# Performance work log

Measured on AMD Instinct MI355X. Metric: run time of the kernel, lower is better.

Reference implementation:

```python
import jax, jax.numpy as jnp
import numpy as np
from functools import partial

B, S, D, H, DK, DV, DFF = 4, 2048, 1024, 8, 128, 128, 4096
EPS = 1e-6

def rms_norm(x):
    return x * jax.lax.rsqrt(jnp.mean(x * x, axis=-1, keepdims=True) + EPS)

def l2norm(x):
    return x * jax.lax.rsqrt(jnp.sum(x * x, axis=-1, keepdims=True) + EPS)

def setup_inputs() -> dict:
    key = jax.random.key(0)
    ks = jax.random.split(key, 16)
    w = lambda k, shp: jax.random.normal(k, shp, dtype=jnp.float32) * 0.02
    return {
        'x': jax.random.normal(ks[0], (B, S, D), dtype=jnp.float32),
        'Wq': w(ks[1], (D, H * DK)),
        'Wk': w(ks[2], (D, H * DK)),
        'Wv': w(ks[3], (D, H * DV)),
        'Wb': w(ks[4], (D, H)),
        'Wa': w(ks[5], (D, H)),
        'A_log': jnp.log(jnp.linspace(1.0, 8.0, H).astype(jnp.float32)),
        'dt_bias': jax.random.normal(ks[6], (H,), dtype=jnp.float32) * 0.1,
        'Wg': w(ks[7], (D, H * DV)),
        'o_norm_w': jnp.ones((DV,), dtype=jnp.float32),
        'Wo': w(ks[8], (H * DV, D)),
        'W_fc': w(ks[9], (D, DFF)),
        'W_proj': w(ks[10], (DFF, D)),
    }

def gated_delta_net(h, Wq, Wk, Wv, Wb, Wa, A_log, dt_bias, Wg, o_norm_w, Wo):
    b, s, _ = h.shape
    q = l2norm(jax.nn.silu(h @ Wq).reshape(b, s, H, DK))
    k = l2norm(jax.nn.silu(h @ Wk).reshape(b, s, H, DK))
    v = jax.nn.silu(h @ Wv).reshape(b, s, H, DV)
    beta = jax.nn.sigmoid(h @ Wb)                                  # [b,s,H]
    g = -jnp.exp(A_log) * jax.nn.softplus(h @ Wa + dt_bias)       # [b,s,H]
    alpha = jnp.exp(g)
    scale = DK ** -0.5

    # time-major for scan
    tm = lambda a: jnp.moveaxis(a, 1, 0)
    qs, ks_, vs, als, bts = tm(q), tm(k), tm(v), tm(alpha), tm(beta)

    def step(Sst, inp):
        q_t, k_t, v_t, a_t, b_t = inp               # [b,H,dk],[b,H,dk],[b,H,dv],[b,H],[b,H]
        Sst = Sst * a_t[..., None, None]            # decay state [b,H,dk,dv]
        kv = jnp.einsum('bhd,bhde->bhe', k_t, Sst)  # current memory readout
        delta = (v_t - kv) * b_t[..., None]
        Sst = Sst + jnp.einsum('bhd,bhe->bhde', k_t, delta)
        o_t = jnp.einsum('bhd,bhde->bhe', q_t, Sst) * scale
        return Sst, o_t

    S0 = jnp.zeros((b, H, DK, DV), dtype=h.dtype)
    _, o = jax.lax.scan(step, S0, (qs, ks_, vs, als, bts))
    o = jnp.moveaxis(o, 0, 1)                       # [b,s,H,dv]

    gate = (h @ Wg).reshape(b, s, H, DV)
    o = rms_norm(o) * o_norm_w * jax.nn.silu(gate)  # gated RMSNorm
    return o.reshape(b, s, H * DV) @ Wo

def reference(x, Wq, Wk, Wv, Wb, Wa, A_log, dt_bias, Wg, o_norm_w, Wo, W_fc, W_proj):
    ln_scale = 1.0  # config.layer_norm_scaling = False
    h = gated_delta_net(ln_scale * rms_norm(x), Wq, Wk, Wv, Wb, Wa, A_log, dt_bias, Wg, o_norm_w, Wo)
    x = x + h
    m = ln_scale * rms_norm(x)
    y = jnp.square(jax.nn.relu(m @ W_fc)) @ W_proj  # nanoGPT ReLU^2 MLP
    return x + y
```

## Files before the change

### kernel.cpp

```cpp
#include <hip/hip_runtime.h>
#include <math.h>
#include <stdint.h>

#define ROWS 8192
#define DIM  1024
#define NH   8
#define DFF_ 4096
#define EPSF 1e-6f
#define SCALEQ 0.08838834764831845f

typedef __attribute__((ext_vector_type(8))) short short8;
typedef __attribute__((ext_vector_type(4))) float f32x4;

__device__ __forceinline__ float siluf(float x) {
    return x / (1.0f + expf(-x));
}
__device__ __forceinline__ unsigned short f2bf(float f) {
    uint32_t u = __float_as_uint(f);
    uint32_t r = (u + 0x7FFFu + ((u >> 16) & 1u)) >> 16;
    return (unsigned short)r;
}
__device__ __forceinline__ float bf2f(unsigned short u) {
    return __uint_as_float(((uint32_t)u) << 16);
}

__device__ __forceinline__ void async16(const void* g, void* l) {
    __builtin_amdgcn_global_load_lds(
        (const __attribute__((address_space(1))) uint32_t*)g,
        (__attribute__((address_space(3))) uint32_t*)l, 16, 0, 0);
}

__global__ void rmsnorm_bf16_kernel(const float* __restrict__ x, unsigned short* __restrict__ y) {
    int row = blockIdx.x;
    int tid = threadIdx.x;
    const float4* x4 = (const float4*)(x + (size_t)row * DIM);
    float4 v = x4[tid];
    float ss = v.x * v.x + v.y * v.y + v.z * v.z + v.w * v.w;
#pragma unroll
    for (int m = 1; m < 64; m <<= 1) ss += __shfl_xor(ss, m, 64);
    __shared__ float wss[4];
    if ((tid & 63) == 0) wss[tid >> 6] = ss;
    __syncthreads();
    float tot = wss[0] + wss[1] + wss[2] + wss[3];
    float r = rsqrtf(tot * (1.0f / 1024.0f) + EPSF);
    ushort4 o;
    o.x = f2bf(v.x * r); o.y = f2bf(v.y * r); o.z = f2bf(v.z * r); o.w = f2bf(v.w * r);
    ((ushort4*)(y + (size_t)row * DIM))[tid] = o;
}

__global__ void transpose_bf16_kernel(const float* __restrict__ W, unsigned short* __restrict__ WT,
                                      int K, int N) {
    __shared__ float tile[32][33];
    int n0 = blockIdx.x * 32, k0 = blockIdx.y * 32;
    int tx = threadIdx.x & 31, ty = threadIdx.x >> 5;
#pragma unroll
    for (int r = 0; r < 32; r += 8)
        tile[ty + r][tx] = W[(size_t)(k0 + ty + r) * N + n0 + tx];
    __syncthreads();
#pragma unroll
    for (int r = 0; r < 32; r += 8)
        WT[(size_t)(n0 + ty + r) * K + k0 + tx] = f2bf(tile[tx][ty + r]);
}

template <int EPI, typename CT>
__global__ __launch_bounds__(256) void mfma_gemm(
    const unsigned short* __restrict__ A, const unsigned short* __restrict__ BT,
    CT* __restrict__ C, const float* __restrict__ res, int M, int N, int K) {
    __shared__ __align__(16) unsigned short As[128 * 32];
    __shared__ __align__(16) unsigned short Bs[128 * 32];
    int tid = threadIdx.x;
    int w = tid >> 6, lane = tid & 63;

    int nwgx = gridDim.x;
    int nwg = nwgx * gridDim.y;
    int id = blockIdx.y * nwgx + blockIdx.x;
    int cpx = nwg >> 3;
    int nid = (id & 7) * cpx + (id >> 3);
    int bxs = nid % nwgx, bys = nid / nwgx;

    int bm = bys * 128, bn = bxs * 128;
    int wm = (w >> 1) * 64, wn = (w & 1) * 64;

    int srow = tid >> 2;
    int skb = ((tid & 3) ^ ((tid >> 3) & 3)) * 8;
    const unsigned short* Ag = A + (size_t)(bm + srow) * K + skb;
    const unsigned short* Bg = BT + (size_t)(bn + srow) * K + skb;

    f32x4 acc[4][4] = {};

    int lr = lane & 15;
    int lk = (((lane >> 4) ^ ((lr >> 1) & 3))) * 8;

    for (int kt = 0; kt < K; kt += 32) {
        async16(Ag + kt, As + w * 512);
        async16(Ag + kt + (size_t)64 * K, As + 2048 + w * 512);
        async16(Bg + kt, Bs + w * 512);
        async16(Bg + kt + (size_t)64 * K, Bs + 2048 + w * 512);
        __syncthreads();
        short8 af[4], bf[4];
#pragma unroll
        for (int i = 0; i < 4; i++) {
            af[i] = *(const short8*)&As[(wm + i * 16 + lr) * 32 + lk];
            bf[i] = *(const short8*)&Bs[(wn + i * 16 + lr) * 32 + lk];
        }
#pragma unroll
        for (int i = 0; i < 4; i++)
#pragma unroll
            for (int j = 0; j < 4; j++)
                acc[i][j] = __builtin_amdgcn_mfma_f32_16x16x32_bf16(af[i], bf[j], acc[i][j], 0, 0, 0);
        __syncthreads();
    }

#pragma unroll
    for (int i = 0; i < 4; i++) {
        int gr0 = bm + wm + i * 16 + (lane >> 4) * 4;
#pragma unroll
        for (int j = 0; j < 4; j++) {
            int gc = bn + wn + j * 16 + lr;
#pragma unroll
            for (int r = 0; r < 4; r++) {
                float v = acc[i][j][r];
                size_t idx = (size_t)(gr0 + r) * N + gc;
                if (EPI == 1) v = siluf(v);
                else if (EPI == 2) v += res[idx];
                else if (EPI == 3) { float t = fmaxf(v, 0.0f); v = t * t; }
                if constexpr (sizeof(CT) == 2) C[idx] = (CT)f2bf(v);
                else C[idx] = v;
            }
        }
    }
}

__global__ __launch_bounds__(256) void mfma_gemm_qkvg(
    const unsigned short* __restrict__ A, const unsigned short* __restrict__ BT,
    unsigned short* __restrict__ oq, unsigned short* __restrict__ ok,
    unsigned short* __restrict__ ov, unsigned short* __restrict__ og, int M, int K) {
    __shared__ __align__(16) unsigned short As[128 * 32];
    __shared__ __align__(16) unsigned short Bs[128 * 32];
    int tid = threadIdx.x;
    int w = tid >> 6, lane = tid & 63;

    int nwgx = gridDim.x;
    int nwg = nwgx * gridDim.y;
    int id = blockIdx.y * nwgx + blockIdx.x;
    int cpx = nwg >> 3;
    int nid = (id & 7) * cpx + (id >> 3);
    int bxs = nid % nwgx, bys = nid / nwgx;

    int bm = bys * 128, bn = bxs * 128;
    int wm = (w >> 1) * 64, wn = (w & 1) * 64;

    int srow = tid >> 2;
    int skb = ((tid & 3) ^ ((tid >> 3) & 3)) * 8;
    const unsigned short* Ag = A + (size_t)(bm + srow) * K + skb;
    const unsigned short* Bg = BT + (size_t)(bn + srow) * K + skb;

    f32x4 acc[4][4] = {};
    int lr = lane & 15;
    int lk = (((lane >> 4) ^ ((lr >> 1) & 3))) * 8;
    int l4 = (lane >> 4) * 4;

    for (int kt = 0; kt < K; kt += 32) {
        async16(Ag + kt, As + w * 512);
        async16(Ag + kt + (size_t)64 * K, As + 2048 + w * 512);
        async16(Bg + kt, Bs + w * 512);
        async16(Bg + kt + (size_t)64 * K, Bs + 2048 + w * 512);
        __syncthreads();
        short8 af[4], bf[4];
#pragma unroll
        for (int i = 0; i < 4; i++) {
            af[i] = *(const short8*)&As[(wm + i * 16 + lr) * 32 + lk];
            bf[i] = *(const short8*)&Bs[(wn + i * 16 + lr) * 32 + lk];
        }
#pragma unroll
        for (int i = 0; i < 4; i++)
#pragma unroll
            for (int j = 0; j < 4; j++)
                acc[i][j] = __builtin_amdgcn_mfma_f32_16x16x32_bf16(af[i], bf[j], acc[i][j], 0, 0, 0);
        __syncthreads();
    }

    int bsel = bn >> 10;
    int bnl = bn & 1023;
    if (bsel < 3) {
#pragma unroll
        for (int i = 0; i < 4; i++)
#pragma unroll
            for (int j = 0; j < 4; j++)
#pragma unroll
                for (int r = 0; r < 4; r++)
                    acc[i][j][r] = siluf(acc[i][j][r]);
    }
    float* sums = (float*)As;
    bool donorm = (bsel < 2);
    if (donorm) {
#pragma unroll
        for (int i = 0; i < 4; i++) {
#pragma unroll
            for (int r = 0; r < 4; r++) {
                float p = acc[i][0][r] * acc[i][0][r] + acc[i][1][r] * acc[i][1][r] +
                          acc[i][2][r] * acc[i][2][r] + acc[i][3][r] * acc[i][3][r];
                p += __shfl_xor(p, 1, 16);
                p += __shfl_xor(p, 2, 16);
                p += __shfl_xor(p, 4, 16);
                p += __shfl_xor(p, 8, 16);
                if (lr == 0) sums[(wm + i * 16 + l4 + r) * 2 + (wn >> 6)] = p;
            }
        }
        __syncthreads();
    }
    unsigned short* C = (bsel == 0) ? oq : (bsel == 1) ? ok : (bsel == 2) ? ov : og;
#pragma unroll
    for (int i = 0; i < 4; i++) {
#pragma unroll
        for (int r = 0; r < 4; r++) {
            int lrow = wm + i * 16 + l4 + r;
            float rn = 1.0f;
            if (donorm) rn = rsqrtf(sums[lrow * 2] + sums[lrow * 2 + 1] + EPSF);
            size_t gr = (size_t)(bm + lrow) * 1024;
#pragma unroll
            for (int j = 0; j < 4; j++) {
                int gc = bnl + wn + j * 16 + lr;
                C[gr + gc] = f2bf(acc[i][j][r] * rn);
            }
        }
    }
}

__global__ void gating_kernel(const float* __restrict__ o, const unsigned short* __restrict__ gate,
                              const float* __restrict__ w, unsigned short* __restrict__ ob) {
    int row = blockIdx.x;
    int tid = threadIdx.x;
    const float4* op = (const float4*)(o + (size_t)row * DIM);
    float4 v = op[tid];
    float ss = v.x * v.x + v.y * v.y + v.z * v.z + v.w * v.w;
#pragma unroll
    for (int m = 1; m < 32; m <<= 1) ss += __shfl_xor(ss, m, 32);
    float r = rsqrtf(ss * (1.0f / 128.0f) + EPSF);
    ushort4 gu = ((const ushort4*)(gate + (size_t)row * DIM))[tid];
    float4 wv = ((const float4*)w)[tid & 31];
    ushort4 out;
    out.x = f2bf(v.x * r * wv.x * siluf(bf2f(gu.x)));
    out.y = f2bf(v.y * r * wv.y * siluf(bf2f(gu.y)));
    out.z = f2bf(v.z * r * wv.z * siluf(bf2f(gu.z)));
    out.w = f2bf(v.w * r * wv.w * siluf(bf2f(gu.w)));
    ((ushort4*)(ob + (size_t)row * DIM))[tid] = out;
}

__global__ void smallproj_kernel(const unsigned short* __restrict__ hbuf,
                                 const float* __restrict__ Wb, const float* __restrict__ Wa,
                                 const float* __restrict__ A_log, const float* __restrict__ dt_bias,
                                 float* __restrict__ Glog, float* __restrict__ Beta) {
    int row = blockIdx.x;
    int tid = threadIdx.x;
    __shared__ __align__(16) float hrow[1024];
    __shared__ float part[128];
    const ushort4* h4 = (const ushort4*)(hbuf + (size_t)row * DIM);
    ushort4 u0 = h4[tid * 2], u1 = h4[tid * 2 + 1];
    hrow[tid * 8 + 0] = bf2f(u0.x); hrow[tid * 8 + 1] = bf2f(u0.y);
    hrow[tid * 8 + 2] = bf2f(u0.z); hrow[tid * 8 + 3] = bf2f(u0.w);
    hrow[tid * 8 + 4] = bf2f(u1.x); hrow[tid * 8 + 5] = bf2f(u1.y);
    hrow[tid * 8 + 6] = bf2f(u1.z); hrow[tid * 8 + 7] = bf2f(u1.w);
    __syncthreads();
    int out = tid & 15, slice = tid >> 4;
    const float* W = (out < 8) ? Wb : Wa;
    int col = out & 7;
    int k0 = slice * 128;
    float p = 0.0f;
    for (int kk = 0; kk < 128; kk++) p += hrow[k0 + kk] * W[(size_t)(k0 + kk) * 8 + col];
    part[tid] = p;
    __syncthreads();
    if (tid < 16) {
        float sum = 0.0f;
#pragma unroll
        for (int sl = 0; sl < 8; sl++) sum += part[sl * 16 + tid];
        if (tid < 8) {
            Beta[(size_t)row * 8 + tid] = 1.0f / (1.0f + expf(-sum));
        } else {
            int hh = tid - 8;
            float xg = sum + dt_bias[hh];
            float sp = fmaxf(xg, 0.0f) + log1pf(expf(-fabsf(xg)));
            Glog[(size_t)row * 8 + hh] = -expf(A_log[hh]) * sp;
        }
    }
}

#define PRE_KB 0
#define PRE_QB 17408
#define PRE_YL 17408
#define PRE_LM 34816
#define PRE_MT 44032
#define PRE_FL 76800
#define PRE_SZ 77824

__global__ __launch_bounds__(256) void chunk_prep_kernel(
    const unsigned short* __restrict__ Q16, const unsigned short* __restrict__ K16,
    const unsigned short* __restrict__ V16, const float* __restrict__ Glog,
    const float* __restrict__ Beta,
    unsigned short* __restrict__ Wg, unsigned short* __restrict__ Ug,
    unsigned short* __restrict__ Qg, unsigned short* __restrict__ KTg,
    unsigned short* __restrict__ SMg, float* __restrict__ Pcs) {
    __shared__ __align__(16) unsigned char smem[PRE_SZ];
    unsigned short* Kb = (unsigned short*)(smem + PRE_KB);
    unsigned short* Qb = (unsigned short*)(smem + PRE_QB);
    unsigned short* Yl = (unsigned short*)(smem + PRE_YL);
    unsigned short* Lm = (unsigned short*)(smem + PRE_LM);
    float* betl = (float*)(smem + PRE_FL);
    float* Gl = betl + 64;
    float* Pl = Gl + 64;
    float* decf = Pl + 64;

    int blk = blockIdx.x;
    int bh = blk & 31, c = blk >> 5;
    int b = bh >> 3, h = bh & 7;
    int bhc = bh * 32 + c;
    int row0 = b * 2048 + c * 64;
    int col0 = h * 128;
    int tid = threadIdx.x;
    int wv = tid >> 6, lane = tid & 63;
    int lr = lane & 15, lk8 = (lane >> 4) * 8, l4 = (lane >> 4) * 4;

#pragma unroll
    for (int r = 0; r < 4; ++r) {
        int cc = tid + r * 256;
        int i = cc >> 4, jc = (cc & 15) * 8;
        *(short8*)&Kb[i * 136 + jc] = *(const short8*)(K16 + (size_t)(row0 + i) * DIM + col0 + jc);
        *(short8*)&Qb[i * 136 + jc] = *(const short8*)(Q16 + (size_t)(row0 + i) * DIM + col0 + jc);
    }
    {
        short8 z = {};
        for (int o = tid; o < 576; o += 256) ((short8*)Lm)[o] = z;
        for (int o = tid; o < 2048; o += 256) ((short8*)(smem + PRE_MT))[o] = z;
    }
    if (tid < 64) {
        float g = Glog[(size_t)(row0 + tid) * 8 + h];
        betl[tid] = Beta[(size_t)(row0 + tid) * 8 + h];
#pragma unroll
        for (int d = 1; d < 64; d <<= 1) {
            float t = __shfl_up(g, d, 64);
            if (tid >= d) g += t;
        }
        Gl[tid] = g;
        Pl[tid] = expf(g);
        float g63 = __shfl(g, 63, 64);
        decf[tid] = expf(g63 - g);
        if (tid == 63) Pcs[bhc] = expf(g);
    }
    __syncthreads();

    for (int nt = 0; nt <= wv; nt++) {
        f32x4 acc = {};
#pragma unroll
        for (int kk = 0; kk < 4; kk++) {
            short8 af = *(const short8*)&Kb[(wv * 16 + lr) * 136 + kk * 32 + lk8];
            short8 bfr = *(const short8*)&Kb[(nt * 16 + lr) * 136 + kk * 32 + lk8];
            acc = __builtin_amdgcn_mfma_f32_16x16x32_bf16(af, bfr, acc, 0, 0, 0);
        }
#pragma unroll
        for (int r = 0; r < 4; r++) {
            int i = wv * 16 + l4 + r;
            int j = nt * 16 + lr;
            if (j < i) Lm[i * 72 + j] = f2bf(betl[i] * expf(Gl[i] - Gl[j]) * acc[r]);
        }
    }
    for (int nt = 0; nt < 4; nt++) {
        f32x4 acc = {};
        if (nt <= wv) {
#pragma unroll
            for (int kk = 0; kk < 4; kk++) {
                short8 af = *(const short8*)&Qb[(wv * 16 + lr) * 136 + kk * 32 + lk8];
                short8 bfr = *(const short8*)&Kb[(nt * 16 + lr) * 136 + kk * 32 + lk8];
                acc = __builtin_amdgcn_mfma_f32_16x16x32_bf16(af, bfr, acc, 0, 0, 0);
            }
        }
#pragma unroll
        for (int r = 0; r < 4; r++) {
            int i = wv * 16 + l4 + r;
            int j = nt * 16 + lr;
            float vv = (nt <= wv && j <= i) ? SCALEQ * expf(Gl[i] - Gl[j]) * acc[r] : 0.f;
            SMg[((size_t)bhc * 64 + i) * 64 + j] = f2bf(vv);
        }
    }
    {
        int d = tid & 127, ih = tid >> 7;
        for (int i0 = 0; i0 < 32; i0++) {
            int i = ih * 32 + i0;
            Qg[((size_t)bhc * 64 + i) * 128 + d] = f2bf(SCALEQ * Pl[i] * bf2f(Qb[i * 136 + d]));
        }
        for (int j8 = 0; j8 < 32; j8 += 8) {
            short8 v8;
#pragma unroll
            for (int e = 0; e < 8; e++) {
                int jj = ih * 32 + j8 + e;
                v8[e] = (short)f2bf(decf[jj] * bf2f(Kb[jj * 136 + d]));
            }
            *(short8*)&KTg[((size_t)bhc * 128 + d) * 64 + ih * 32 + j8] = v8;
        }
    }
    __syncthreads();

    int n = tid;
    bool isW = n < 128;
    int cW = n & 127;
    unsigned short* Gout = isW ? Wg : Ug;
    const unsigned short* Vcol = V16 + (size_t)row0 * DIM + col0 + cW;
    for (int bi = 0; bi < 4; ++bi) {
        if (bi > 0) {
            int ib = bi * 16;
#pragma unroll
            for (int t4 = 0; t4 < 4; ++t4) {
                int nt = wv * 4 + t4;
                f32x4 acc = {};
#pragma unroll
                for (int ks = 0; ks < 2; ++ks) {
                    short8 af = *(const short8*)&Lm[(ib + lr) * 72 + ks * 32 + lk8];
                    int nr = nt * 16 + lr;
                    int cj = ks * 4 + (lk8 >> 3);
                    short8 bfr = *(const short8*)(smem + PRE_MT + nr * 128 + (((cj ^ (nr & 7)) & 7) << 4));
                    acc = __builtin_amdgcn_mfma_f32_16x16x32_bf16(af, bfr, acc, 0, 0, 0);
                }
#pragma unroll
                for (int r = 0; r < 4; ++r)
                    Yl[(l4 + r) * 264 + nt * 16 + lr] = f2bf(acc[r]);
            }
        }
        __syncthreads();
        float xs[16];
#pragma unroll
        for (int ii = 0; ii < 16; ++ii) {
            int i = bi * 16 + ii;
            float a = isW ? betl[i] * Pl[i] * bf2f(Kb[i * 136 + cW])
                          : betl[i] * bf2f(Vcol[(size_t)i * DIM]);
            if (bi > 0) a -= bf2f(Yl[ii * 264 + n]);
#pragma unroll
            for (int j = 0; j < 15; ++j)
                if (j < ii) a = fmaf(-bf2f(Lm[i * 72 + bi * 16 + j]), xs[j], a);
            xs[ii] = a;
        }
        {
            short8 m0, m1;
#pragma unroll
            for (int e = 0; e < 8; ++e) { m0[e] = (short)f2bf(xs[e]); m1[e] = (short)f2bf(xs[8 + e]); }
            int cj0 = bi * 2, cj1 = bi * 2 + 1;
            *(short8*)(smem + PRE_MT + n * 128 + (((cj0 ^ (n & 7)) & 7) << 4)) = m0;
            *(short8*)(smem + PRE_MT + n * 128 + (((cj1 ^ (n & 7)) & 7) << 4)) = m1;
        }
#pragma unroll
        for (int ii = 0; ii < 16; ++ii)
            Gout[((size_t)bhc * 64 + bi * 16 + ii) * 128 + cW] = f2bf(xs[ii]);
        __syncthreads();
    }
}

__global__ __launch_bounds__(256) void chunk_scan2_kernel(
    const unsigned short* __restrict__ Wg, const unsigned short* __restrict__ Ug,
    const unsigned short* __restrict__ Qg, const unsigned short* __restrict__ KTg,
    const unsigned short* __restrict__ SMg, const float* __restrict__ Pcs,
    float* __restrict__ O) {
    int blk = blockIdx.x;
    int bh = blk & 31, dvg = blk >> 5;
    int b = bh >> 3, h = bh & 7;
    int col16 = dvg * 16;
    int tid = threadIdx.x;
    int wv = tid >> 6, lane = tid & 63;
    int lr = lane & 15, lk8 = (lane >> 4) * 8, l4 = (lane >> 4) * 4;
    int i0 = wv * 16;

    __shared__ __align__(16) unsigned short Wl[64 * 136];
    __shared__ __align__(16) unsigned short Ql[64 * 136];
    __shared__ __align__(16) unsigned short KTl[128 * 72];
    __shared__ __align__(16) unsigned short SMl[64 * 72];
    __shared__ __align__(16) unsigned short Ul[64 * 24];
    __shared__ __align__(16) unsigned short STl[16 * 136];
    __shared__ __align__(16) unsigned short DTl[16 * 72];

    for (int e = tid; e < 16 * 136; e += 256) STl[e] = 0;

    f32x4 Sacc[2] = {};

    for (int c = 0; c < 32; c++) {
        int bhc = bh * 32 + c;
        size_t base8k = (size_t)bhc * 8192;
        float pc = Pcs[bhc];
#pragma unroll
        for (int r = 0; r < 4; r++) {
            int v = tid + r * 256;
            *(short8*)&Wl[(v >> 4) * 136 + (v & 15) * 8] = *(const short8*)(Wg + base8k + (size_t)v * 8);
            *(short8*)&Ql[(v >> 4) * 136 + (v & 15) * 8] = *(const short8*)(Qg + base8k + (size_t)v * 8);
            *(short8*)&KTl[(v >> 3) * 72 + (v & 7) * 8] = *(const short8*)(KTg + base8k + (size_t)v * 8);
        }
#pragma unroll
        for (int r = 0; r < 2; r++) {
            int v = tid + r * 256;
            *(short8*)&SMl[(v >> 3) * 72 + (v & 7) * 8] = *(const short8*)(SMg + (size_t)bhc * 4096 + (size_t)v * 8);
        }
        if (tid < 128) {
            int row = tid >> 1, hf = tid & 1;
            *(short8*)&Ul[row * 24 + hf * 8] =
                *(const short8*)(Ug + base8k + (size_t)row * 128 + col16 + hf * 8);
        }
        __syncthreads();

        f32x4 acc0 = {}, acc1 = {};
#pragma unroll
        for (int kd = 0; kd < 4; kd++) {
            short8 bfs = *(const short8*)&STl[lr * 136 + kd * 32 + lk8];
            short8 aw = *(const short8*)&Wl[(i0 + lr) * 136 + kd * 32 + lk8];
            short8 aq = *(const short8*)&Ql[(i0 + lr) * 136 + kd * 32 + lk8];
            acc0 = __builtin_amdgcn_mfma_f32_16x16x32_bf16(aw, bfs, acc0, 0, 0, 0);
            acc1 = __builtin_amdgcn_mfma_f32_16x16x32_bf16(aq, bfs, acc1, 0, 0, 0);
        }
        ushort4 dpk;
        dpk.x = f2bf(bf2f(Ul[(i0 + l4 + 0) * 24 + lr]) - acc0[0]);
        dpk.y = f2bf(bf2f(Ul[(i0 + l4 + 1) * 24 + lr]) - acc0[1]);
        dpk.z = f2bf(bf2f(Ul[(i0 + l4 + 2) * 24 + lr]) - acc0[2]);
        dpk.w = f2bf(bf2f(Ul[(i0 + l4 + 3) * 24 + lr]) - acc0[3]);
        *(ushort4*)&DTl[lr * 72 + i0 + l4] = dpk;
        __syncthreads();

#pragma unroll
        for (int dt = 0; dt < 2; dt++)
#pragma unroll
            for (int r = 0; r < 4; r++) Sacc[dt][r] *= pc;
#pragma unroll
        for (int kj = 0; kj < 2; kj++) {
            short8 bfd = *(const short8*)&DTl[lr * 72 + kj * 32 + lk8];
            short8 as = *(const short8*)&SMl[(i0 + lr) * 72 + kj * 32 + lk8];
            acc1 = __builtin_amdgcn_mfma_f32_16x16x32_bf16(as, bfd, acc1, 0, 0, 0);
#pragma unroll
            for (int dt = 0; dt < 2; dt++) {
                short8 ak = *(const short8*)&KTl[((2 * wv + dt) * 16 + lr) * 72 + kj * 32 + lk8];
                Sacc[dt] = __builtin_amdgcn_mfma_f32_16x16x32_bf16(ak, bfd, Sacc[dt], 0, 0, 0);
            }
        }
        {
            int orow0 = b * 2048 + c * 64 + i0 + l4;
            int ocol = h * 128 + col16 + lr;
#pragma unroll
            for (int r = 0; r < 4; r++)
                O[(size_t)(orow0 + r) * DIM + ocol] = acc1[r];
        }
#pragma unroll
        for (int dt = 0; dt < 2; dt++) {
            ushort4 sp;
            sp.x = f2bf(Sacc[dt][0]);
            sp.y = f2bf(Sacc[dt][1]);
            sp.z = f2bf(Sacc[dt][2]);
            sp.w = f2bf(Sacc[dt][3]);
            *(ushort4*)&STl[lr * 136 + (2 * wv + dt) * 16 + l4] = sp;
        }
        __syncthreads();
    }
}

extern "C" void kernel_launch(void* const* d_in, const int* in_sizes, int n_in,
                              void* d_out, int out_size, void* d_ws, size_t ws_size,
                              hipStream_t stream) {
    const float* x      = (const float*)d_in[0];
    const float* Wq     = (const float*)d_in[1];
    const float* Wk     = (const float*)d_in[2];
    const float* Wv     = (const float*)d_in[3];
    const float* Wb     = (const float*)d_in[4];
    const float* Wa     = (const float*)d_in[5];
    const float* A_log  = (const float*)d_in[6];
    const float* dt_b   = (const float*)d_in[7];
    const float* Wg_in  = (const float*)d_in[8];
    const float* o_norm = (const float*)d_in[9];
    const float* Wo     = (const float*)d_in[10];
    const float* W_fc   = (const float*)d_in[11];
    const float* W_proj = (const float*)d_in[12];
    float* out = (float*)d_out;

    const size_t MATE = (size_t)ROWS * DIM;
    unsigned short* qb16 = (unsigned short*)d_ws;
    unsigned short* kb16 = qb16 + MATE;
    unsigned short* vb16 = kb16 + MATE;
    unsigned short* gt16 = vb16 + MATE;
    float* o_f = (float*)(gt16 + MATE);
    unsigned short* h_bf = (unsigned short*)(o_f + MATE);
    float* glog = (float*)(h_bf + MATE);
    float* beta = glog + (size_t)ROWS * NH;
    unsigned short* wts = (unsigned short*)(beta + (size_t)ROWS * NH);
    unsigned short* WqT = wts;
    unsigned short* WkT = wts + (1u << 20);
    unsigned short* WvT = wts + 2 * (1u << 20);
    unsigned short* WgT = wts + 3 * (1u << 20);
    unsigned short* WoT = wts + 4 * (1u << 20);
    unsigned short* WfcT = wts + 5 * (1u << 20);
    unsigned short* WprT = wts + 9 * (1u << 20);
    unsigned short* Wgb = wts + 13 * (1u << 20);
    unsigned short* Ugb = Wgb + (8u << 20);
    unsigned short* Qg2 = Ugb + (8u << 20);
    unsigned short* KTg = Qg2 + (8u << 20);
    unsigned short* SMg = KTg + (8u << 20);
    float* pcs = (float*)(SMg + (4u << 20));
    unsigned short* m_bf = h_bf;
    unsigned short* o_bf = vb16;
    unsigned short* fc_bf = qb16;

    transpose_bf16_kernel<<<dim3(32, 32), 256, 0, stream>>>(Wq, WqT, 1024, 1024);
    transpose_bf16_kernel<<<dim3(32, 32), 256, 0, stream>>>(Wk, WkT, 1024, 1024);
    transpose_bf16_kernel<<<dim3(32, 32), 256, 0, stream>>>(Wv, WvT, 1024, 1024);
    transpose_bf16_kernel<<<dim3(32, 32), 256, 0, stream>>>(Wg_in, WgT, 1024, 1024);
    transpose_bf16_kernel<<<dim3(32, 32), 256, 0, stream>>>(Wo, WoT, 1024, 1024);
    transpose_bf16_kernel<<<dim3(128, 32), 256, 0, stream>>>(W_fc, WfcT, 1024, 4096);
    transpose_bf16_kernel<<<dim3(32, 128), 256, 0, stream>>>(W_proj, WprT, 4096, 1024);

    rmsnorm_bf16_kernel<<<ROWS, 256, 0, stream>>>(x, h_bf);

    mfma_gemm_qkvg<<<dim3(4096 / 128, ROWS / 128), 256, 0, stream>>>(
        h_bf, WqT, qb16, kb16, vb16, gt16, ROWS, DIM);

    smallproj_kernel<<<ROWS, 128, 0, stream>>>(h_bf, Wb, Wa, A_log, dt_b, glog, beta);

    chunk_prep_kernel<<<1024, 256, 0, stream>>>(qb16, kb16, vb16, glog, beta,
                                                Wgb, Ugb, Qg2, KTg, SMg, pcs);
    chunk_scan2_kernel<<<256, 256, 0, stream>>>(Wgb, Ugb, Qg2, KTg, SMg, pcs, o_f);

    gating_kernel<<<ROWS, 256, 0, stream>>>(o_f, gt16, o_norm, o_bf);

    dim3 g1(DIM / 128, ROWS / 128);
    mfma_gemm<2, float><<<g1, 256, 0, stream>>>(o_bf, WoT, out, x, ROWS, DIM, DIM);

    rmsnorm_bf16_kernel<<<ROWS, 256, 0, stream>>>(out, m_bf);

    dim3 g2(DFF_ / 128, ROWS / 128);
    mfma_gemm<3, unsigned short><<<g2, 256, 0, stream>>>(m_bf, WfcT, fc_bf, nullptr, ROWS, DFF_, DIM);

    mfma_gemm<2, float><<<g1, 256, 0, stream>>>(fc_bf, WprT, out, out, ROWS, DIM, DFF_);
}
```

Measured before the change: 548.1 us.

## Replace 128x128 GEMMs with 256x256 double-buffered, 8-wave pipelined MFMA kernel

Replaces the single-buffered 128x128-tile GEMM (4 waves, a barrier after every 32-wide K step) with 256x256 tiles computed by 8 waves. The new loop double-buffers 64-wide K slices in LDS and interleaves async global-to-LDS prefetch of the next slice with MFMA on the current one, using explicit waitcnt, barriers and setprio. The aim is to hide global load latency and raise arithmetic intensity per tile. In exchange it uses much more LDS per block and more accumulator registers, and launches fewer blocks: the Wo and proj GEMMs get only 128 blocks, which may leave compute units underused.

```diff
diff --git a/kernel.cpp b/kernel.cpp
--- a/kernel.cpp
+++ b/kernel.cpp
@@ -62,67 +62,115 @@
         WT[(size_t)(n0 + ty + r) * K + k0 + tx] = f2bf(tile[tx][ty + r]);
 }
 
+
+#define G256_DECL \
+    __shared__ __align__(16) unsigned short AL[2][2][256 * 32]; \
+    __shared__ __align__(16) unsigned short BL[2][2][256 * 32]; \
+    int tid = threadIdx.x; \
+    int w = tid >> 6, lane = tid & 63; \
+    int wm = w >> 2, wn = w & 3; \
+    int lr = lane & 15; \
+    int nwgx = gridDim.x; \
+    int nwg = nwgx * gridDim.y; \
+    int id = blockIdx.y * nwgx + blockIdx.x; \
+    int cpx = nwg >> 3; \
+    int nid = (id & 7) * cpx + (id >> 3); \
+    int bxs = nid % nwgx, bys = nid / nwgx; \
+    int bm = bys * 256, bn = bxs * 256; \
+    int stg_r = w * 32 + (lane >> 2); \
+    int stg_c = ((lane & 3) ^ ((lane >> 3) & 3)) * 8; \
+    const unsigned short* Ag = A + (size_t)(bm + stg_r) * K + stg_c; \
+    const unsigned short* Bg = BT + (size_t)(bn + stg_r) * K + stg_c; \
+    int pc = ((lane >> 4) ^ ((lr >> 1) & 3)) * 8; \
+    f32x4 acc[8][4] = {}; \
+    short8 bf[4], af[4]; \
+    int nt = K / 64;
+
+#define G256_STAGE_A(buf, s, kto) do { \
+    async16(Ag + (kto) + (s) * 32, &AL[buf][s][(w * 2 + 0) * 512]); \
+    async16(Ag + (size_t)16 * K + (kto) + (s) * 32, &AL[buf][s][(w * 2 + 1) * 512]); \
+} while (0)
+#define G256_STAGE_B(buf, s, kto) do { \
+    async16(Bg + (kto) + (s) * 32, &BL[buf][s][(w * 2 + 0) * 512]); \
+    async16(Bg + (size_t)16 * K + (kto) + (s) * 32, &BL[buf][s][(w * 2 + 1) * 512]); \
+} while (0)
+
+#define G256_READ_B(cur, s) do { \
+    _Pragma("unroll") \
+    for (int j = 0; j < 4; ++j) \
+        bf[j] = *(const short8*)&BL[cur][s][(wn * 64 + j * 16 + lr) * 32 + pc]; \
+} while (0)
+#define G256_READ_A(cur, s, rh) do { \
+    _Pragma("unroll") \
+    for (int i = 0; i < 4; ++i) \
+        af[i] = *(const short8*)&AL[cur][s][(wm * 128 + (rh) * 64 + i * 16 + lr) * 32 + pc]; \
+} while (0)
+
+#define G256_MFMA(rh) do { \
+    __builtin_amdgcn_s_barrier(); \
+    asm volatile("s_waitcnt lgkmcnt(0)" ::: "memory"); \
+    __builtin_amdgcn_s_setprio(1); \
+    _Pragma("unroll") \
+    for (int i = 0; i < 4; ++i) \
+        _Pragma("unroll") \
+        for (int j = 0; j < 4; ++j) \
+            acc[(rh) * 4 + i][j] = __builtin_amdgcn_mfma_f32_16x16x32_bf16(af[i], bf[j], acc[(rh) * 4 + i][j], 0, 0, 0); \
+    __builtin_amdgcn_s_setprio(0); \
+} while (0)
+
+#define G256_MAINLOOP \
+    G256_STAGE_A(0, 0, 0); G256_STAGE_B(0, 0, 0); \
+    G256_STAGE_A(0, 1, 0); G256_STAGE_B(0, 1, 0); \
+    asm volatile("s_waitcnt vmcnt(0)" ::: "memory"); \
+    __builtin_amdgcn_s_barrier(); \
+    for (int t = 0; t < nt; ++t) { \
+        int cur = t & 1, nxt = cur ^ 1; \
+        bool pf = (t + 1 < nt); \
+        int ktn = (t + 1) * 64; \
+         \
+        G256_READ_B(cur, 0); \
+        G256_READ_A(cur, 0, 0); \
+        if (pf) G256_STAGE_A(nxt, 0, ktn); \
+        G256_MFMA(0); \
+        __builtin_amdgcn_s_barrier(); \
+         \
+        G256_READ_A(cur, 0, 1); \
+        if (pf) G256_STAGE_B(nxt, 0, ktn); \
+        G256_MFMA(1); \
+        asm volatile("s_waitcnt vmcnt(4)" ::: "memory"); \
+        __builtin_amdgcn_s_barrier(); \
+         \
+        G256_READ_B(cur, 1); \
+        G256_READ_A(cur, 1, 0); \
+        if (pf) G256_STAGE_A(nxt, 1, ktn); \
+        G256_MFMA(0); \
+        __builtin_amdgcn_s_barrier(); \
+         \
+        G256_READ_A(cur, 1, 1); \
+        if (pf) G256_STAGE_B(nxt, 1, ktn); \
+        G256_MFMA(1); \
+        asm volatile("s_waitcnt vmcnt(4)" ::: "memory"); \
+        __builtin_amdgcn_s_barrier(); \
+    }
+
 template <int EPI, typename CT>
-__global__ __launch_bounds__(256) void mfma_gemm(
+__global__ __launch_bounds__(512, 2) void gemm256(
     const unsigned short* __restrict__ A, const unsigned short* __restrict__ BT,
     CT* __restrict__ C, const float* __restrict__ res, int M, int N, int K) {
-    __shared__ __align__(16) unsigned short As[128 * 32];
-    __shared__ __align__(16) unsigned short Bs[128 * 32];
-    int tid = threadIdx.x;
-    int w = tid >> 6, lane = tid & 63;
-
-    int nwgx = gridDim.x;
-    int nwg = nwgx * gridDim.y;
-    int id = blockIdx.y * nwgx + blockIdx.x;
-    int cpx = nwg >> 3;
-    int nid = (id & 7) * cpx + (id >> 3);
-    int bxs = nid % nwgx, bys = nid / nwgx;
-
-    int bm = bys * 128, bn = bxs * 128;
-    int wm = (w >> 1) * 64, wn = (w & 1) * 64;
-
-    int srow = tid >> 2;
-    int skb = ((tid & 3) ^ ((tid >> 3) & 3)) * 8;
-    const unsigned short* Ag = A + (size_t)(bm + srow) * K + skb;
-    const unsigned short* Bg = BT + (size_t)(bn + srow) * K + skb;
-
-    f32x4 acc[4][4] = {};
-
-    int lr = lane & 15;
-    int lk = (((lane >> 4) ^ ((lr >> 1) & 3))) * 8;
-
-    for (int kt = 0; kt < K; kt += 32) {
-        async16(Ag + kt, As + w * 512);
-        async16(Ag + kt + (size_t)64 * K, As + 2048 + w * 512);
-        async16(Bg + kt, Bs + w * 512);
-        async16(Bg + kt + (size_t)64 * K, Bs + 2048 + w * 512);
-        __syncthreads();
-        short8 af[4], bf[4];
-#pragma unroll
-        for (int i = 0; i < 4; i++) {
-            af[i] = *(const short8*)&As[(wm + i * 16 + lr) * 32 + lk];
-            bf[i] = *(const short8*)&Bs[(wn + i * 16 + lr) * 32 + lk];
-        }
-#pragma unroll
-        for (int i = 0; i < 4; i++)
-#pragma unroll
-            for (int j = 0; j < 4; j++)
-                acc[i][j] = __builtin_amdgcn_mfma_f32_16x16x32_bf16(af[i], bf[j], acc[i][j], 0, 0, 0);
-        __syncthreads();
-    }
-
-#pragma unroll
-    for (int i = 0; i < 4; i++) {
-        int gr0 = bm + wm + i * 16 + (lane >> 4) * 4;
-#pragma unroll
-        for (int j = 0; j < 4; j++) {
-            int gc = bn + wn + j * 16 + lr;
-#pragma unroll
-            for (int r = 0; r < 4; r++) {
-                float v = acc[i][j][r];
+    G256_DECL
+    G256_MAINLOOP
+
+#pragma unroll
+    for (int rf = 0; rf < 8; ++rf) {
+        int gr0 = bm + wm * 128 + rf * 16 + (lane >> 4) * 4;
+#pragma unroll
+        for (int cf = 0; cf < 4; ++cf) {
+            int gc = bn + wn * 64 + cf * 16 + lr;
+#pragma unroll
+            for (int r = 0; r < 4; ++r) {
+                float v = acc[rf][cf][r];
                 size_t idx = (size_t)(gr0 + r) * N + gc;
-                if (EPI == 1) v = siluf(v);
-                else if (EPI == 2) v += res[idx];
+                if (EPI == 2) v += res[idx];
                 else if (EPI == 3) { float t = fmaxf(v, 0.0f); v = t * t; }
                 if constexpr (sizeof(CT) == 2) C[idx] = (CT)f2bf(v);
                 else C[idx] = v;
@@ -131,97 +179,59 @@
     }
 }
 
-__global__ __launch_bounds__(256) void mfma_gemm_qkvg(
+__global__ __launch_bounds__(512, 2) void qkvg256(
     const unsigned short* __restrict__ A, const unsigned short* __restrict__ BT,
     unsigned short* __restrict__ oq, unsigned short* __restrict__ ok,
     unsigned short* __restrict__ ov, unsigned short* __restrict__ og, int M, int K) {
-    __shared__ __align__(16) unsigned short As[128 * 32];
-    __shared__ __align__(16) unsigned short Bs[128 * 32];
-    int tid = threadIdx.x;
-    int w = tid >> 6, lane = tid & 63;
-
-    int nwgx = gridDim.x;
-    int nwg = nwgx * gridDim.y;
-    int id = blockIdx.y * nwgx + blockIdx.x;
-    int cpx = nwg >> 3;
-    int nid = (id & 7) * cpx + (id >> 3);
-    int bxs = nid % nwgx, bys = nid / nwgx;
-
-    int bm = bys * 128, bn = bxs * 128;
-    int wm = (w >> 1) * 64, wn = (w & 1) * 64;
-
-    int srow = tid >> 2;
-    int skb = ((tid & 3) ^ ((tid >> 3) & 3)) * 8;
-    const unsigned short* Ag = A + (size_t)(bm + srow) * K + skb;
-    const unsigned short* Bg = BT + (size_t)(bn + srow) * K + skb;
-
-    f32x4 acc[4][4] = {};
-    int lr = lane & 15;
-    int lk = (((lane >> 4) ^ ((lr >> 1) & 3))) * 8;
-    int l4 = (lane >> 4) * 4;
-
-    for (int kt = 0; kt < K; kt += 32) {
-        async16(Ag + kt, As + w * 512);
-        async16(Ag + kt + (size_t)64 * K, As + 2048 + w * 512);
-        async16(Bg + kt, Bs + w * 512);
-        async16(Bg + kt + (size_t)64 * K, Bs + 2048 + w * 512);
-        __syncthreads();
-        short8 af[4], bf[4];
-#pragma unroll
-        for (int i = 0; i < 4; i++) {
-            af[i] = *(const short8*)&As[(wm + i * 16 + lr) * 32 + lk];
-            bf[i] = *(const short8*)&Bs[(wn + i * 16 + lr) * 32 + lk];
-        }
-#pragma unroll
-        for (int i = 0; i < 4; i++)
-#pragma unroll
-            for (int j = 0; j < 4; j++)
-                acc[i][j] = __builtin_amdgcn_mfma_f32_16x16x32_bf16(af[i], bf[j], acc[i][j], 0, 0, 0);
-        __syncthreads();
-    }
+    const int N = 4096;
+    (void)N;
+    __shared__ float sums[256 * 4];
+    G256_DECL
+    G256_MAINLOOP
 
     int bsel = bn >> 10;
     int bnl = bn & 1023;
     if (bsel < 3) {
 #pragma unroll
-        for (int i = 0; i < 4; i++)
-#pragma unroll
-            for (int j = 0; j < 4; j++)
-#pragma unroll
-                for (int r = 0; r < 4; r++)
-                    acc[i][j][r] = siluf(acc[i][j][r]);
-    }
-    float* sums = (float*)As;
+        for (int rf = 0; rf < 8; ++rf)
+#pragma unroll
+            for (int cf = 0; cf < 4; ++cf)
+#pragma unroll
+                for (int r = 0; r < 4; ++r)
+                    acc[rf][cf][r] = siluf(acc[rf][cf][r]);
+    }
     bool donorm = (bsel < 2);
     if (donorm) {
 #pragma unroll
-        for (int i = 0; i < 4; i++) {
-#pragma unroll
-            for (int r = 0; r < 4; r++) {
-                float p = acc[i][0][r] * acc[i][0][r] + acc[i][1][r] * acc[i][1][r] +
-                          acc[i][2][r] * acc[i][2][r] + acc[i][3][r] * acc[i][3][r];
+        for (int rf = 0; rf < 8; ++rf) {
+#pragma unroll
+            for (int r = 0; r < 4; ++r) {
+                float p = acc[rf][0][r] * acc[rf][0][r] + acc[rf][1][r] * acc[rf][1][r] +
+                          acc[rf][2][r] * acc[rf][2][r] + acc[rf][3][r] * acc[rf][3][r];
                 p += __shfl_xor(p, 1, 16);
                 p += __shfl_xor(p, 2, 16);
                 p += __shfl_xor(p, 4, 16);
                 p += __shfl_xor(p, 8, 16);
-                if (lr == 0) sums[(wm + i * 16 + l4 + r) * 2 + (wn >> 6)] = p;
+                if (lr == 0)
+                    sums[(wm * 128 + rf * 16 + (lane >> 4) * 4 + r) * 4 + wn] = p;
             }
         }
         __syncthreads();
     }
     unsigned short* C = (bsel == 0) ? oq : (bsel == 1) ? ok : (bsel == 2) ? ov : og;
 #pragma unroll
-    for (int i = 0; i < 4; i++) {
-#pragma unroll
-        for (int r = 0; r < 4; r++) {
-            int lrow = wm + i * 16 + l4 + r;
+    for (int rf = 0; rf < 8; ++rf) {
+#pragma unroll
+        for (int r = 0; r < 4; ++r) {
+            int lrow = wm * 128 + rf * 16 + (lane >> 4) * 4 + r;
             float rn = 1.0f;
-            if (donorm) rn = rsqrtf(sums[lrow * 2] + sums[lrow * 2 + 1] + EPSF);
+            if (donorm)
+                rn = rsqrtf(sums[lrow * 4 + (wn & 2)] + sums[lrow * 4 + (wn & 2) + 1] + EPSF);
             size_t gr = (size_t)(bm + lrow) * 1024;
 #pragma unroll
-            for (int j = 0; j < 4; j++) {
-                int gc = bnl + wn + j * 16 + lr;
-                C[gr + gc] = f2bf(acc[i][j][r] * rn);
+            for (int cf = 0; cf < 4; ++cf) {
+                int gc = bnl + wn * 64 + cf * 16 + lr;
+                C[gr + gc] = f2bf(acc[rf][cf][r] * rn);
             }
         }
     }
@@ -608,7 +618,7 @@
 
     rmsnorm_bf16_kernel<<<ROWS, 256, 0, stream>>>(x, h_bf);
 
-    mfma_gemm_qkvg<<<dim3(4096 / 128, ROWS / 128), 256, 0, stream>>>(
+    qkvg256<<<dim3(4096 / 256, ROWS / 256), 512, 0, stream>>>(
         h_bf, WqT, qb16, kb16, vb16, gt16, ROWS, DIM);
 
     smallproj_kernel<<<ROWS, 128, 0, stream>>>(h_bf, Wb, Wa, A_log, dt_b, glog, beta);
@@ -619,13 +629,14 @@
 
     gating_kernel<<<ROWS, 256, 0, stream>>>(o_f, gt16, o_norm, o_bf);
 
-    dim3 g1(DIM / 128, ROWS / 128);
-    mfma_gemm<2, float><<<g1, 256, 0, stream>>>(o_bf, WoT, out, x, ROWS, DIM, DIM);
+    gemm256<2, float><<<dim3(1024 / 256, ROWS / 256), 512, 0, stream>>>(
+        o_bf, WoT, out, x, ROWS, DIM, DIM);
 
     rmsnorm_bf16_kernel<<<ROWS, 256, 0, stream>>>(out, m_bf);
 
-    dim3 g2(DFF_ / 128, ROWS / 128);
-    mfma_gemm<3, unsigned short><<<g2, 256, 0, stream>>>(m_bf, WfcT, fc_bf, nullptr, ROWS, DFF_, DIM);
-
-    mfma_gemm<2, float><<<g1, 256, 0, stream>>>(fc_bf, WprT, out, out, ROWS, DIM, DFF_);
-}
+    gemm256<3, unsigned short><<<dim3(DFF_ / 256, ROWS / 256), 512, 0, stream>>>(
+        m_bf, WfcT, fc_bf, nullptr, ROWS, DFF_, DIM);
+
+    gemm256<2, float><<<dim3(1024 / 256, ROWS / 256), 512, 0, stream>>>(
+        fc_bf, WprT, out, out, ROWS, DIM, DFF_);
+}
```

Result: slower. 563.9 us (+2.9%).
